# Kernel optimization log

Hardware: AMD Instinct MI355X
Metric: run time of the kernel (lower is better)

The kernel has to match this reference:

```python
import jax, jax.numpy as jnp
import numpy as np

EMB_DIM = 1024
ATT_DIM = 1024

def setup_inputs() -> dict:
    key = jax.random.key(0)
    ks = jax.random.split(key, 7)
    B, S = 8, 2048
    x_h = jax.random.normal(ks[0], (B, S, EMB_DIM), dtype=jnp.float32)
    # Linear params (stored as [in, out] for x @ W + b)
    sq = 1.0 / np.sqrt(EMB_DIM)
    Wq = jax.random.uniform(ks[1], (EMB_DIM, ATT_DIM), jnp.float32, -sq, sq)
    bq = jax.random.uniform(ks[2], (ATT_DIM,), jnp.float32, -sq, sq)
    Wk = jax.random.uniform(ks[3], (EMB_DIM, ATT_DIM), jnp.float32, -sq, sq)
    bk = jax.random.uniform(ks[4], (ATT_DIM,), jnp.float32, -sq, sq)
    Wv = jax.random.uniform(ks[5], (EMB_DIM, EMB_DIM), jnp.float32, -sq, sq)
    bv = jax.random.uniform(ks[6], (EMB_DIM,), jnp.float32, -sq, sq)
    return {"x_h": x_h, "Wq": Wq, "bq": bq, "Wk": Wk, "bk": bk, "Wv": Wv, "bv": bv}

def reference(x_h, Wq, bq, Wk, bk, Wv, bv):
    q = x_h @ Wq + bq               # [B,S,att_dim]
    k = x_h @ Wk + bk               # [B,S,att_dim]
    v = x_h @ Wv + bv               # [B,S,emb_dim]
    scale = 1.0 / jnp.sqrt(jnp.asarray(k.shape[-1], q.dtype))
    scores = jnp.einsum('bqd,bkd->bqk', q, k) * scale   # [B,S,S]
    # NOTE: original softmaxes over dim=1 (the QUERY axis), not the key axis.
    attn = jax.nn.softmax(scores, axis=1)
    return jnp.einsum('bqk,bkd->bqd', attn, v)
```

## Files before the change

kernel.cpp:

```cpp
#include <hip/hip_runtime.h>
#include <math.h>

typedef __bf16 bf16x8 __attribute__((ext_vector_type(8)));
typedef float f32x4 __attribute__((ext_vector_type(4)));
typedef unsigned short ushort8 __attribute__((ext_vector_type(8)));
typedef unsigned short ushort4v __attribute__((ext_vector_type(4)));
typedef unsigned short u16;

#define DEVINL __device__ __forceinline__

DEVINL u16 f2bf(float f) {
    union { float f; unsigned u; } a; a.f = f;
    unsigned u = a.u;
    return (u16)((u + 0x7FFFu + ((u >> 16) & 1u)) >> 16);
}
DEVINL float bf2f(u16 h) { return __uint_as_float(((unsigned)h) << 16); }

DEVINL void gload_lds16(const void* g, void* l) {
    __builtin_amdgcn_global_load_lds(
        (__attribute__((address_space(1))) void*)(g),
        (__attribute__((address_space(3))) void*)(l),
        16, 0, 0);
}

template<int EPI>
__global__ __launch_bounds__(512, 2)
void gemm256(const u16* __restrict__ A, int lda, long sAz,
             const u16* __restrict__ B, int ldb, long sBz,
             void* __restrict__ Cv, int ldc, long sCz,
             const float* __restrict__ bias, float* __restrict__ part,
             float scale, int K)
{
    __shared__ u16 lds[65536];
    const int tid = threadIdx.x;
    const int tile_x = blockIdx.x, tile_y = blockIdx.y;
    const long bz = blockIdx.z;

    const u16* Ab = A + bz * sAz;
    const u16* Bb = B + bz * sBz;
    const int row0 = tile_x * 256, col0 = tile_y * 256;

    const int sr = tid >> 2;
    const int csw = ((tid & 3) * 16) ^ (((sr >> 1) & 3) << 4);
    const u16* Ag = Ab + (long)(row0 + sr) * lda + (csw >> 1);
    const u16* Bg = Bb + (long)(col0 + sr) * ldb + (csw >> 1);
    const int dst0 = tid * 8;

    const int lane = tid & 63, wid = tid >> 6;
    const int wm = wid >> 2, wn = wid & 3;
    const int lane_r = lane & 15;
    const int rdcol = (((lane >> 4) * 16) ^ (((lane_r >> 1) & 3) << 4)) >> 1;
    const int arow0 = wm * 128 + lane_r;
    const int brow0 = wn * 64 + lane_r;

    const int NT = K >> 6;
    f32x4 acc[8][4] = {};
    bf16x8 af[4], bfrag[4];

    auto issueA = [&](int t1, int s, int buf) {
        const u16* g = Ag + (long)t1 * 64 + s * 32;
        u16* d = &lds[(buf * 2 + s) * 8192 + dst0];
        gload_lds16(g, d);
        gload_lds16(g + (long)128 * lda, d + 4096);
    };
    auto issueB = [&](int t1, int s, int buf) {
        const u16* g = Bg + (long)t1 * 64 + s * 32;
        u16* d = &lds[32768 + (buf * 2 + s) * 8192 + dst0];
        gload_lds16(g, d);
        gload_lds16(g + (long)128 * ldb, d + 4096);
    };

#define READ_A(s, h)                                                        \
    _Pragma("unroll")                                                       \
    for (int m = 0; m < 4; ++m)                                             \
        af[m] = *(const bf16x8*)&lds[(buf * 2 + (s)) * 8192 +               \
                     (arow0 + (h) * 64 + m * 16) * 32 + rdcol];

#define READ_B(s)                                                           \
    _Pragma("unroll")                                                       \
    for (int n = 0; n < 4; ++n)                                             \
        bfrag[n] = *(const bf16x8*)&lds[32768 + (buf * 2 + (s)) * 8192 +    \
                     (brow0 + n * 16) * 32 + rdcol];

#define MFMA16(h)                                                           \
    __builtin_amdgcn_s_setprio(1);                                          \
    _Pragma("unroll")                                                       \
    for (int m = 0; m < 4; ++m)                                             \
        _Pragma("unroll")                                                   \
        for (int n = 0; n < 4; ++n)                                         \
            acc[(h) * 4 + m][n] = __builtin_amdgcn_mfma_f32_16x16x32_bf16(  \
                bfrag[n], af[m], acc[(h) * 4 + m][n], 0, 0, 0);             \
    __builtin_amdgcn_s_setprio(0);

#define GATE(n)                                                             \
    asm volatile("s_waitcnt vmcnt(" #n ")" ::: "memory");                   \
    __builtin_amdgcn_s_barrier();

    issueA(0, 0, 0); issueB(0, 0, 0); issueA(0, 1, 0); issueB(0, 1, 0);
    GATE(4);

    for (int t = 0; t < NT - 1; ++t) {
        const int buf = t & 1, nbuf = buf ^ 1;
        READ_A(0, 0); READ_B(0);
        issueA(t + 1, 0, nbuf);
        MFMA16(0);
        READ_A(0, 1);
        issueB(t + 1, 0, nbuf);
        MFMA16(1);
        GATE(4);
        READ_A(1, 0); READ_B(1);
        issueA(t + 1, 1, nbuf);
        MFMA16(0);
        READ_A(1, 1);
        issueB(t + 1, 1, nbuf);
        MFMA16(1);
        GATE(4);
    }
    {
        const int buf = (NT - 1) & 1;
        READ_A(0, 0); READ_B(0);
        MFMA16(0);
        READ_A(0, 1);
        MFMA16(1);
        GATE(0);
        READ_A(1, 0); READ_B(1);
        MFMA16(0);
        READ_A(1, 1);
        MFMA16(1);
    }
#undef READ_A
#undef READ_B
#undef MFMA16
#undef GATE

    const int erow = lane & 15, ecol0 = (lane >> 4) * 4;
    float4 bias4[4];
    if constexpr (EPI == 0) {
#pragma unroll
        for (int nf = 0; nf < 4; ++nf)
            bias4[nf] = *(const float4*)&bias[col0 + wn * 64 + nf * 16 + ecol0];
    }
    f32x4 csum[4] = {};
#pragma unroll
    for (int mf = 0; mf < 8; ++mf) {
        const int gr = row0 + wm * 128 + mf * 16 + erow;
#pragma unroll
        for (int nf = 0; nf < 4; ++nf) {
            const int gc = col0 + wn * 64 + nf * 16 + ecol0;
            f32x4 v = acc[mf][nf];
            if constexpr (EPI == 0) {
                v[0] += bias4[nf].x; v[1] += bias4[nf].y;
                v[2] += bias4[nf].z; v[3] += bias4[nf].w;
                ushort4v o = { f2bf(v[0]), f2bf(v[1]), f2bf(v[2]), f2bf(v[3]) };
                *(ushort4v*)((u16*)Cv + bz * sCz + (long)gr * ldc + gc) = o;
            } else if constexpr (EPI == 1) {
                f32x4 e;
#pragma unroll
                for (int r = 0; r < 4; ++r) e[r] = __expf(v[r] * scale);
                csum[nf] += e;
                ushort4v o = { f2bf(e[0]), f2bf(e[1]), f2bf(e[2]), f2bf(e[3]) };
                *(ushort4v*)((u16*)Cv + bz * sCz + (long)gr * ldc + gc) = o;
            } else {
                *(float4*)((float*)Cv + bz * sCz + (long)gr * ldc + gc) =
                    make_float4(v[0], v[1], v[2], v[3]);
            }
        }
    }
    if constexpr (EPI == 1) {
#pragma unroll
        for (int nf = 0; nf < 4; ++nf)
#pragma unroll
            for (int r = 0; r < 4; ++r) {
                float s = csum[nf][r];
                s += __shfl_xor(s, 1);
                s += __shfl_xor(s, 2);
                s += __shfl_xor(s, 4);
                s += __shfl_xor(s, 8);
                csum[nf][r] = s;
            }
        if ((lane & 15) == 0) {
#pragma unroll
            for (int nf = 0; nf < 4; ++nf) {
                float* p = part + ((bz * 16 + (long)tile_x * 2 + wm) * 2048)
                         + col0 + wn * 64 + nf * 16 + ecol0;
                *(float4*)p = make_float4(csum[nf][0], csum[nf][1],
                                          csum[nf][2], csum[nf][3]);
            }
        }
    }
}

__global__ void cast_x_k(const float* __restrict__ x, u16* __restrict__ o)
{
    const int i = blockIdx.x * 256 + threadIdx.x;
    const float4* xv = (const float4*)x;
    const float4 a = xv[(long)i * 2], b = xv[(long)i * 2 + 1];
    ushort8 r;
    r[0] = f2bf(a.x); r[1] = f2bf(a.y); r[2] = f2bf(a.z); r[3] = f2bf(a.w);
    r[4] = f2bf(b.x); r[5] = f2bf(b.y); r[6] = f2bf(b.z); r[7] = f2bf(b.w);
    *(ushort8*)(o + (long)i * 8) = r;
}

__global__ void wt_k(const float* __restrict__ Wq, const float* __restrict__ Wk,
                     const float* __restrict__ Wv, u16* __restrict__ Wt)
{
    __shared__ float t[32][33];
    const int z = blockIdx.z;
    const float* W = (z == 0) ? Wq : ((z == 1) ? Wk : Wv);
    const int k0 = blockIdx.x * 32, n0 = blockIdx.y * 32;
    const int tx = threadIdx.x, ty = threadIdx.y;
#pragma unroll
    for (int j = 0; j < 32; j += 8)
        t[ty + j][tx] = W[(long)(k0 + ty + j) * 1024 + n0 + tx];
    __syncthreads();
#pragma unroll
    for (int j = 0; j < 32; j += 8)
        Wt[((long)z * 1024 + n0 + ty + j) * 1024 + k0 + tx] = f2bf(t[tx][ty + j]);
}

__global__ void bias_k(const float* __restrict__ bq, const float* __restrict__ bk,
                       const float* __restrict__ bv, float* __restrict__ bcat)
{
    const int i = blockIdx.x * 256 + threadIdx.x;
    bcat[i] = (i < 1024) ? bq[i] : ((i < 2048) ? bk[i - 1024] : bv[i - 2048]);
}

__global__ void rcp_k(const float* __restrict__ part, float* __restrict__ rden)
{
    const int b = blockIdx.y;
    const int k = blockIdx.x * 256 + threadIdx.x;
    float s = 0.f;
#pragma unroll
    for (int c = 0; c < 16; ++c) s += part[((long)b * 16 + c) * 2048 + k];
    rden[b * 2048 + k] = 1.0f / s;
}

__global__ void vt_k(const u16* __restrict__ qkv, const float* __restrict__ rden,
                     u16* __restrict__ Vt)
{
    __shared__ float t[32][33];
    const int b = blockIdx.z;
    const int k0 = blockIdx.x * 32, d0 = blockIdx.y * 32;
    const int tx = threadIdx.x, ty = threadIdx.y;
#pragma unroll
    for (int j = 0; j < 32; j += 8) {
        const int k = k0 + ty + j;
        t[ty + j][tx] = bf2f(qkv[((long)b * 2048 + k) * 3072 + 2048 + d0 + tx])
                        * rden[b * 2048 + k];
    }
    __syncthreads();
#pragma unroll
    for (int j = 0; j < 32; j += 8)
        Vt[((long)b * 1024 + d0 + ty + j) * 2048 + k0 + tx] = f2bf(t[tx][ty + j]);
}

extern "C" void kernel_launch(void* const* d_in, const int* in_sizes, int n_in,
                              void* d_out, int out_size, void* d_ws, size_t ws_size,
                              hipStream_t stream)
{
    const float* x  = (const float*)d_in[0];
    const float* Wq = (const float*)d_in[1];
    const float* bq = (const float*)d_in[2];
    const float* Wk = (const float*)d_in[3];
    const float* bk = (const float*)d_in[4];
    const float* Wv = (const float*)d_in[5];
    const float* bv = (const float*)d_in[6];

    char* ws = (char*)d_ws;
    u16*   qkv  = (u16*)(ws);
    u16*   E    = (u16*)(ws + 100663296);
    u16*   Vt   = (u16*)(ws + 167772160);
    u16*   xb   = (u16*)(ws + 201326592);
    u16*   Wt   = (u16*)(ws + 234881024);
    float* bcat = (float*)(ws + 241172480);
    float* part = (float*)(ws + 241184768);
    float* rden = (float*)(ws + 243281920);

    const long sQKV = (long)2048 * 3072;
    const long sE   = (long)2048 * 2048;
    const long sVt  = (long)1024 * 2048;
    const long sO   = (long)2048 * 1024;

    cast_x_k<<<8192, 256, 0, stream>>>(x, xb);
    wt_k<<<dim3(32, 32, 3), dim3(32, 8), 0, stream>>>(Wq, Wk, Wv, Wt);
    bias_k<<<12, 256, 0, stream>>>(bq, bk, bv, bcat);
    gemm256<0><<<dim3(64, 12, 1), 512, 0, stream>>>(
        xb, 1024, 0, Wt, 1024, 0, qkv, 3072, 0, bcat, nullptr, 0.f, 1024);
    gemm256<1><<<dim3(8, 8, 8), 512, 0, stream>>>(
        qkv, 3072, sQKV, qkv + 1024, 3072, sQKV, E, 2048, sE,
        nullptr, part, 0.03125f, 1024);
    rcp_k<<<dim3(8, 8), 256, 0, stream>>>(part, rden);
    vt_k<<<dim3(64, 32, 8), dim3(32, 8), 0, stream>>>(qkv, rden, Vt);
    gemm256<2><<<dim3(8, 4, 8), 512, 0, stream>>>(
        E, 2048, sE, Vt, 2048, sVt, d_out, 1024, sO,
        nullptr, nullptr, 1.f, 2048);
}
```

Measured before the change: 303.7 us.

## Double-buffer LDS-to-register fragments to overlap LDS reads with MFMAs

Adds two register fragment sets for A and B and software-pipelines the GEMM main loop. The reads for the next half-tile are issued before the MFMAs on the current set run, and the global-to-LDS prefetches for each stage are now issued together. The aim is to hide LDS read latency behind MFMA work instead of stalling on it. The cost is about 32 more VGPRs per thread, which could lower occupancy, plus a redundant reread of the B fragments for each half.

```diff
diff --git a/kernel.cpp b/kernel.cpp
--- a/kernel.cpp
+++ b/kernel.cpp
@@ -55,82 +55,78 @@
 
     const int NT = K >> 6;
     f32x4 acc[8][4] = {};
-    bf16x8 af[4], bfrag[4];
-
-    auto issueA = [&](int t1, int s, int buf) {
+    bf16x8 aF0[4], bF0[4], aF1[4], bF1[4];
+
+    auto issueA = [&](int t1, int s, int b) {
         const u16* g = Ag + (long)t1 * 64 + s * 32;
-        u16* d = &lds[(buf * 2 + s) * 8192 + dst0];
+        u16* d = &lds[(b * 2 + s) * 8192 + dst0];
         gload_lds16(g, d);
         gload_lds16(g + (long)128 * lda, d + 4096);
     };
-    auto issueB = [&](int t1, int s, int buf) {
+    auto issueB = [&](int t1, int s, int b) {
         const u16* g = Bg + (long)t1 * 64 + s * 32;
-        u16* d = &lds[32768 + (buf * 2 + s) * 8192 + dst0];
+        u16* d = &lds[32768 + (b * 2 + s) * 8192 + dst0];
         gload_lds16(g, d);
         gload_lds16(g + (long)128 * ldb, d + 4096);
     };
 
-#define READ_A(s, h)                                                        \
+#define READ_AB(bufv, s, h, SET)                                            \
     _Pragma("unroll")                                                       \
     for (int m = 0; m < 4; ++m)                                             \
-        af[m] = *(const bf16x8*)&lds[(buf * 2 + (s)) * 8192 +               \
-                     (arow0 + (h) * 64 + m * 16) * 32 + rdcol];
-
-#define READ_B(s)                                                           \
+        aF##SET[m] = *(const bf16x8*)&lds[((bufv) * 2 + (s)) * 8192 +       \
+                         (arow0 + (h) * 64 + m * 16) * 32 + rdcol];         \
     _Pragma("unroll")                                                       \
     for (int n = 0; n < 4; ++n)                                             \
-        bfrag[n] = *(const bf16x8*)&lds[32768 + (buf * 2 + (s)) * 8192 +    \
-                     (brow0 + n * 16) * 32 + rdcol];
-
-#define MFMA16(h)                                                           \
+        bF##SET[n] = *(const bf16x8*)&lds[32768 + ((bufv) * 2 + (s)) * 8192 \
+                         + (brow0 + n * 16) * 32 + rdcol];
+
+#define MFMA16S(SET, h)                                                     \
     __builtin_amdgcn_s_setprio(1);                                          \
     _Pragma("unroll")                                                       \
     for (int m = 0; m < 4; ++m)                                             \
         _Pragma("unroll")                                                   \
         for (int n = 0; n < 4; ++n)                                         \
             acc[(h) * 4 + m][n] = __builtin_amdgcn_mfma_f32_16x16x32_bf16(  \
-                bfrag[n], af[m], acc[(h) * 4 + m][n], 0, 0, 0);             \
+                bF##SET[n], aF##SET[m], acc[(h) * 4 + m][n], 0, 0, 0);      \
     __builtin_amdgcn_s_setprio(0);
 
 #define GATE(n)                                                             \
     asm volatile("s_waitcnt vmcnt(" #n ")" ::: "memory");                   \
     __builtin_amdgcn_s_barrier();
 
-    issueA(0, 0, 0); issueB(0, 0, 0); issueA(0, 1, 0); issueB(0, 1, 0);
+    issueA(0, 0, 0); issueB(0, 0, 0);
+    issueA(0, 1, 0); issueB(0, 1, 0);
     GATE(4);
+    READ_AB(0, 0, 0, 0);
 
     for (int t = 0; t < NT - 1; ++t) {
         const int buf = t & 1, nbuf = buf ^ 1;
-        READ_A(0, 0); READ_B(0);
-        issueA(t + 1, 0, nbuf);
-        MFMA16(0);
-        READ_A(0, 1);
-        issueB(t + 1, 0, nbuf);
-        MFMA16(1);
+        issueA(t + 1, 0, nbuf); issueB(t + 1, 0, nbuf);
+        READ_AB(buf, 0, 1, 1);
+        MFMA16S(0, 0);
         GATE(4);
-        READ_A(1, 0); READ_B(1);
-        issueA(t + 1, 1, nbuf);
-        MFMA16(0);
-        READ_A(1, 1);
-        issueB(t + 1, 1, nbuf);
-        MFMA16(1);
+        READ_AB(buf, 1, 0, 0);
+        MFMA16S(1, 1);
+        issueA(t + 1, 1, nbuf); issueB(t + 1, 1, nbuf);
+        READ_AB(buf, 1, 1, 1);
+        MFMA16S(0, 0);
         GATE(4);
+        READ_AB(nbuf, 0, 0, 0);
+        MFMA16S(1, 1);
     }
     {
         const int buf = (NT - 1) & 1;
-        READ_A(0, 0); READ_B(0);
-        MFMA16(0);
-        READ_A(0, 1);
-        MFMA16(1);
+        READ_AB(buf, 0, 1, 1);
+        MFMA16S(0, 0);
         GATE(0);
-        READ_A(1, 0); READ_B(1);
-        MFMA16(0);
-        READ_A(1, 1);
-        MFMA16(1);
-    }
-#undef READ_A
-#undef READ_B
-#undef MFMA16
+        READ_AB(buf, 1, 0, 0);
+        MFMA16S(1, 1);
+        READ_AB(buf, 1, 1, 1);
+        MFMA16S(0, 0);
+        MFMA16S(1, 1);
+    }
+#undef READ_AB
+#undef MFMA16S
 #undef GATE
 
     const int erow = lane & 15, ecol0 = (lane >> 4) * 4;
```

Result: no change. 301.0 us (-0.9%).
